# Kernel optimization log

Measured on AMD Instinct MI355X. Metric: run time of the kernel, lower is better.

The kernel has to match this reference:

```python
import jax, jax.numpy as jnp
import numpy as np

N = 40000          # nodes
E = 640000         # edges (avg degree 16)
D_MODEL = 128
H = 8              # num_heads
DH = 16            # d_head
DFF = 512
CLAMP = 5.0
EPS = 1e-5


def setup_inputs() -> dict:
    key = jax.random.key(0)
    ks = jax.random.split(key, 10)
    s = 0.08  # weight init scale
    return {
        "feat": jax.random.normal(ks[0], (N, D_MODEL), dtype=jnp.float32),
        "src": jax.random.randint(ks[1], (E,), 0, N, dtype=jnp.int32),
        "dst": jax.random.randint(ks[2], (E,), 0, N, dtype=jnp.int32),
        "Wq": jax.random.normal(ks[3], (H * DH, D_MODEL), dtype=jnp.float32) * s,
        "Wk": jax.random.normal(ks[4], (H * DH, D_MODEL), dtype=jnp.float32) * s,
        "Wv": jax.random.normal(ks[5], (H * DH, D_MODEL), dtype=jnp.float32) * s,
        "Wo": jax.random.normal(ks[6], (D_MODEL, H * DH), dtype=jnp.float32) * s,
        "ln1_g": jnp.ones((D_MODEL,), jnp.float32),
        "ln1_b": jnp.zeros((D_MODEL,), jnp.float32),
        "W1": jax.random.normal(ks[7], (DFF, D_MODEL), dtype=jnp.float32) * s,
        "b1": jnp.zeros((DFF,), jnp.float32),
        "W2": jax.random.normal(ks[8], (D_MODEL, DFF), dtype=jnp.float32) * s,
        "b2": jnp.zeros((D_MODEL,), jnp.float32),
        "ln2_g": jnp.ones((D_MODEL,), jnp.float32),
        "ln2_b": jnp.zeros((D_MODEL,), jnp.float32),
    }


def _layer_norm(x, g, b):
    mu = jnp.mean(x, axis=-1, keepdims=True)
    var = jnp.mean(jnp.square(x - mu), axis=-1, keepdims=True)
    return (x - mu) * jax.lax.rsqrt(var + EPS) * g + b


def reference(feat, src, dst, Wq, Wk, Wv, Wo, ln1_g, ln1_b, W1, b1, W2, b2, ln2_g, ln2_b):
    n = feat.shape[0]
    # Node-level projections (equivalent to DGL's per-edge Linear on gathered feats)
    q = (feat @ Wq.T).reshape(n, H, DH)
    k = (feat @ Wk.T).reshape(n, H, DH)
    v = (feat @ Wv.T).reshape(n, H, DH)

    # Per-edge multi-head attention logits: q[dst] . k[src] / sqrt(d_head), clamped
    u = jnp.sum(q[dst] * k[src], axis=-1) / np.sqrt(DH)   # [E, H]
    u = jnp.clip(u, -CLAMP, CLAMP)

    # Ragged edge-softmax over incoming edges of each dst node
    m = jax.ops.segment_max(u, dst, num_segments=n)        # [N, H]
    e = jnp.exp(u - m[dst])                                # [E, H]
    denom = jax.ops.segment_sum(e, dst, num_segments=n)    # [N, H]
    a = e / denom[dst]                                     # [E, H]

    # Weighted V scatter-reduce back to dst nodes
    av = (a[:, :, None] * v[src]).reshape(-1, H * DH)      # [E, H*DH]
    sum_av = jax.ops.segment_sum(av, dst, num_segments=n)  # [N, H*DH]
    uh = sum_av @ Wo.T                                     # [N, d_model]

    h1 = _layer_norm(feat + uh, ln1_g, ln1_b)
    ffn = jax.nn.relu(h1 @ W1.T + b1) @ W2.T + b2
    return _layer_norm(h1 + ffn, ln2_g, ln2_b)
```

## Files before the change

### kernel.cpp

```cpp
#include <hip/hip_runtime.h>

#define DM 128
#define DFF 512
#define CLAMP_V 5.0f
#define LN_EPS 1e-5f

typedef __attribute__((ext_vector_type(8))) short bf16x8;
typedef __attribute__((ext_vector_type(4))) float f32x4;
typedef __attribute__((ext_vector_type(2))) float f32x2;

__device__ __forceinline__ float b2f(ushort u) {
  union { uint u; float f; } x; x.u = ((uint)u) << 16; return x.f;
}
__device__ __forceinline__ ushort f2b(float f) {
  union { float f; uint u; } x; x.f = f;
  uint r = x.u + 0x7FFFu + ((x.u >> 16) & 1u);
  return (ushort)(r >> 16);
}
__device__ __forceinline__ f32x2 upk2(uint w) {
  union { uint u; float f; } a, b;
  a.u = w << 16; b.u = w & 0xFFFF0000u;
  f32x2 r; r[0] = a.f; r[1] = b.f; return r;
}

__global__ void k_prep(const float* __restrict__ feat,
                       const float* __restrict__ wq, const float* __restrict__ wk,
                       const float* __restrict__ wv, const float* __restrict__ wo,
                       const float* __restrict__ w1, const float* __restrict__ w2,
                       ushort* __restrict__ feat_bf, ushort* __restrict__ wbf,
                       const int* __restrict__ dst, int* __restrict__ deg,
                       int nf4, int castBlocks, int E) {
  if ((int)blockIdx.x >= castBlocks) {
    int e = ((int)blockIdx.x - castBlocks) * 256 + threadIdx.x;
    if (e < E) atomicAdd(&deg[dst[e]], 1);
    return;
  }
  int i = blockIdx.x * 256 + threadIdx.x;
  if (i < nf4) {
    float4 v = *reinterpret_cast<const float4*>(feat + i * 4);
    ushort4 o; o.x = f2b(v.x); o.y = f2b(v.y); o.z = f2b(v.z); o.w = f2b(v.w);
    *reinterpret_cast<ushort4*>(feat_bf + i * 4) = o;
    return;
  }
  int i4 = (i - nf4) * 4;
  if (i4 >= 196608) return;
  const float* s; int o;
  if      (i4 < 16384)  { s = wq; o = i4; }
  else if (i4 < 32768)  { s = wk; o = i4 - 16384; }
  else if (i4 < 49152)  { s = wv; o = i4 - 32768; }
  else if (i4 < 65536)  { s = wo; o = i4 - 49152; }
  else if (i4 < 131072) { s = w1; o = i4 - 65536; }
  else                  { s = w2; o = i4 - 131072; }
  float4 v = *reinterpret_cast<const float4*>(s + o);
  ushort4 u; u.x = f2b(v.x); u.y = f2b(v.y); u.z = f2b(v.z); u.w = f2b(v.w);
  *reinterpret_cast<ushort4*>(wbf + i4) = u;
}

#define SC_EPB 1024

__global__ __launch_bounds__(256) void k_scan(const int* __restrict__ deg,
                                              int* __restrict__ off,
                                              int* __restrict__ cur,
                                              int n, int E) {
  __shared__ int sh[256];
  __shared__ int wsum[4];
  const int t = threadIdx.x;
  const int bstart = blockIdx.x * SC_EPB;

  int gs = 0;
  for (int base = t * 4; base < bstart; base += SC_EPB) {
    int4 v = *reinterpret_cast<const int4*>(deg + base);
    gs += v.x + v.y + v.z + v.w;
  }
  #pragma unroll
  for (int m = 1; m < 64; m <<= 1) gs += __shfl_xor(gs, m);
  if ((t & 63) == 0) wsum[t >> 6] = gs;
  __syncthreads();
  int gadd = wsum[0] + wsum[1] + wsum[2] + wsum[3];
  __syncthreads();

  int base = bstart + t * 4;
  int4 v = {0, 0, 0, 0};
  if (base + 3 < n) {
    v = *reinterpret_cast<const int4*>(deg + base);
  } else {
    if (base     < n) v.x = deg[base];
    if (base + 1 < n) v.y = deg[base + 1];
    if (base + 2 < n) v.z = deg[base + 2];
    if (base + 3 < n) v.w = deg[base + 3];
  }
  int s = v.x + v.y + v.z + v.w;
  sh[t] = s;
  __syncthreads();
  #pragma unroll
  for (int d = 1; d < 256; d <<= 1) {
    int x = 0;
    if (t >= d) x = sh[t - d];
    __syncthreads();
    sh[t] += x;
    __syncthreads();
  }
  int ex = sh[t] - s + gadd;
  if (base + 3 < n) {
    int4 o; o.x = ex; o.y = ex + v.x; o.z = ex + v.x + v.y; o.w = ex + v.x + v.y + v.z;
    *reinterpret_cast<int4*>(off + base) = o;
    int4 z = {0, 0, 0, 0};
    *reinterpret_cast<int4*>(cur + base) = z;
  } else {
    if (base     < n) { off[base]     = ex;                    cur[base]     = 0; }
    if (base + 1 < n) { off[base + 1] = ex + v.x;              cur[base + 1] = 0; }
    if (base + 2 < n) { off[base + 2] = ex + v.x + v.y;        cur[base + 2] = 0; }
    if (base + 3 < n) { off[base + 3] = ex + v.x + v.y + v.z;  cur[base + 3] = 0; }
  }
  if (blockIdx.x == 0 && t == 0) off[n] = E;
}

__global__ void k_scatter(const int* __restrict__ src, const int* __restrict__ dst,
                          const int* __restrict__ off, int* __restrict__ cur,
                          int* __restrict__ csr, int E) {
  int e = blockIdx.x * blockDim.x + threadIdx.x;
  if (e < E) {
    int d = dst[e];
    int p = off[d] + atomicAdd(&cur[d], 1);
    csr[p] = src[e];
  }
}

__global__ __launch_bounds__(512, 2) void k_qkv(
    const ushort* __restrict__ A, const ushort* __restrict__ W,
    ushort* __restrict__ Cb, ushort* __restrict__ Cb2, int M)
{
  __shared__ ushort As[128 * 128];
  __shared__ ushort Bs[128 * 128];

  const int tid = threadIdx.x;
  const int wv = tid >> 6, ln = tid & 63;
  const int bnb = blockIdx.x;
  const int mbase = blockIdx.y * 128;
  const int wrow = (wv >> 2) * 64, wcol = (wv & 3) * 32;
  const int o_base = tid * 16;

  #pragma unroll
  for (int is = 0; is < 4; ++is) {
    int o = is * 8192 + o_base;
    int row = o >> 8;
    int c = ((o >> 4) & 15) ^ (row & 15);
    int gr = min(mbase + row, M - 1);
    const ushort* sA = A + (size_t)gr * 128 + c * 8;
    __builtin_amdgcn_global_load_lds(
        (const __attribute__((address_space(1))) void*)sA,
        (__attribute__((address_space(3))) void*)((char*)As + is * 8192 + wv * 1024),
        16, 0, 0);
    const ushort* sB = W + (size_t)(bnb * 128 + row) * 128 + c * 8;
    __builtin_amdgcn_global_load_lds(
        (const __attribute__((address_space(1))) void*)sB,
        (__attribute__((address_space(3))) void*)((char*)Bs + is * 8192 + wv * 1024),
        16, 0, 0);
  }
  __syncthreads();

  f32x4 acc[4][2] = {};
  const char* AsB = (const char*)As;
  const char* BsB = (const char*)Bs;
  #pragma unroll
  for (int kk = 0; kk < 4; ++kk) {
    bf16x8 af[4], bfr[2];
    #pragma unroll
    for (int m = 0; m < 4; ++m) {
      int r = wrow + m * 16 + (ln & 15);
      int c = kk * 4 + (ln >> 4);
      af[m] = *reinterpret_cast<const bf16x8*>(AsB + r * 256 + ((c ^ (r & 15)) << 4));
    }
    #pragma unroll
    for (int n = 0; n < 2; ++n) {
      int r = wcol + n * 16 + (ln & 15);
      int c = kk * 4 + (ln >> 4);
      bfr[n] = *reinterpret_cast<const bf16x8*>(BsB + r * 256 + ((c ^ (r & 15)) << 4));
    }
    #pragma unroll
    for (int m = 0; m < 4; ++m)
      #pragma unroll
      for (int n = 0; n < 2; ++n)
        acc[m][n] = __builtin_amdgcn_mfma_f32_16x16x32_bf16(af[m], bfr[n], acc[m][n], 0, 0, 0);
  }

  #pragma unroll
  for (int m = 0; m < 4; ++m) {
    int gr0 = mbase + wrow + m * 16 + (ln >> 4) * 4;
    #pragma unroll
    for (int n = 0; n < 2; ++n) {
      int gcl = wcol + n * 16 + (ln & 15);
      #pragma unroll
      for (int r = 0; r < 4; ++r) {
        int gr = gr0 + r;
        if (gr >= M) continue;
        float v = acc[m][n][r];
        if (bnb == 0) Cb[(size_t)gr * 128 + gcl] = f2b(v);
        else          Cb2[(size_t)gr * 256 + (bnb - 1) * 128 + gcl] = f2b(v);
      }
    }
  }
}

__global__ __launch_bounds__(512, 2) void k_mmT(
    const ushort* __restrict__ A, const ushort* __restrict__ W,
    const float* __restrict__ res,
    const float* __restrict__ lng, const float* __restrict__ lnbv,
    ushort* __restrict__ Cb, int M)
{
  __shared__ ushort As[128 * 128];
  __shared__ ushort Bs[128 * 128];
  __shared__ float lnred[1024];

  const int tid = threadIdx.x;
  const int wv = tid >> 6, ln = tid & 63;
  const int mbase = blockIdx.y * 128;
  const int wrow = (wv >> 2) * 64, wcol = (wv & 3) * 32;
  const int o_base = tid * 16;

  #pragma unroll
  for (int is = 0; is < 4; ++is) {
    int o = is * 8192 + o_base;
    int row = o >> 8;
    int c = ((o >> 4) & 15) ^ (row & 15);
    int gr = min(mbase + row, M - 1);
    const ushort* sA = A + (size_t)gr * 128 + c * 8;
    __builtin_amdgcn_global_load_lds(
        (const __attribute__((address_space(1))) void*)sA,
        (__attribute__((address_space(3))) void*)((char*)As + is * 8192 + wv * 1024),
        16, 0, 0);
    const ushort* sB = W + (size_t)row * 128 + c * 8;
    __builtin_amdgcn_global_load_lds(
        (const __attribute__((address_space(1))) void*)sB,
        (__attribute__((address_space(3))) void*)((char*)Bs + is * 8192 + wv * 1024),
        16, 0, 0);
  }
  __syncthreads();

  f32x4 acc[4][2] = {};
  const char* AsB = (const char*)As;
  const char* BsB = (const char*)Bs;
  #pragma unroll
  for (int kk = 0; kk < 4; ++kk) {
    bf16x8 af[4], bfr[2];
    #pragma unroll
    for (int m = 0; m < 4; ++m) {
      int r = wrow + m * 16 + (ln & 15);
      int c = kk * 4 + (ln >> 4);
      af[m] = *reinterpret_cast<const bf16x8*>(AsB + r * 256 + ((c ^ (r & 15)) << 4));
    }
    #pragma unroll
    for (int n = 0; n < 2; ++n) {
      int r = wcol + n * 16 + (ln & 15);
      int c = kk * 4 + (ln >> 4);
      bfr[n] = *reinterpret_cast<const bf16x8*>(BsB + r * 256 + ((c ^ (r & 15)) << 4));
    }
    #pragma unroll
    for (int m = 0; m < 4; ++m)
      #pragma unroll
      for (int n = 0; n < 2; ++n)
        acc[m][n] = __builtin_amdgcn_mfma_f32_16x16x32_bf16(af[m], bfr[n], acc[m][n], 0, 0, 0);
  }

  #pragma unroll
  for (int m = 0; m < 4; ++m)
    #pragma unroll
    for (int n = 0; n < 2; ++n) {
      int gc = wcol + n * 16 + (ln & 15);
      #pragma unroll
      for (int r = 0; r < 4; ++r) {
        int gr = mbase + wrow + m * 16 + (ln >> 4) * 4 + r;
        acc[m][n][r] += res[(size_t)min(gr, M - 1) * 128 + gc];
      }
    }
  #pragma unroll
  for (int m = 0; m < 4; ++m)
    #pragma unroll
    for (int r = 0; r < 4; ++r) {
      float sm = acc[m][0][r] + acc[m][1][r];
      float sq = acc[m][0][r] * acc[m][0][r] + acc[m][1][r] * acc[m][1][r];
      #pragma unroll
      for (int msk = 1; msk <= 8; msk <<= 1) {
        sm += __shfl_xor(sm, msk);
        sq += __shfl_xor(sq, msk);
      }
      if ((ln & 15) == 0) {
        int row = wrow + m * 16 + (ln >> 4) * 4 + r;
        lnred[row * 8 + (wv & 3) * 2]     = sm;
        lnred[row * 8 + (wv & 3) * 2 + 1] = sq;
      }
    }
  __syncthreads();
  #pragma unroll
  for (int m = 0; m < 4; ++m)
    #pragma unroll
    for (int r = 0; r < 4; ++r) {
      int row = wrow + m * 16 + (ln >> 4) * 4 + r;
      int gr = mbase + row;
      float sm = lnred[row * 8] + lnred[row * 8 + 2] + lnred[row * 8 + 4] + lnred[row * 8 + 6];
      float sq = lnred[row * 8 + 1] + lnred[row * 8 + 3] + lnred[row * 8 + 5] + lnred[row * 8 + 7];
      float mu = sm * (1.f / 128.f);
      float var = fmaxf(sq * (1.f / 128.f) - mu * mu, 0.f);
      float rstd = rsqrtf(var + LN_EPS);
      if (gr < M) {
        #pragma unroll
        for (int n = 0; n < 2; ++n) {
          int gc = wcol + n * 16 + (ln & 15);
          float y = (acc[m][n][r] - mu) * rstd * lng[gc] + lnbv[gc];
          Cb[(size_t)gr * 128 + gc] = f2b(y);
        }
      }
    }
}

__global__ __launch_bounds__(512, 4) void k_ffn(
    const ushort* __restrict__ h1b,
    const ushort* __restrict__ w1, const float* __restrict__ b1,
    const ushort* __restrict__ w2, const float* __restrict__ b2,
    const float* __restrict__ lng, const float* __restrict__ lnbv,
    float* __restrict__ outp, int M)
{
  __shared__ ushort mid[32 * 512];
  __shared__ ushort wbuf[2][128 * 64];
  __shared__ float lnred[32 * 16];

  const int tid = threadIdx.x;
  const int wv = tid >> 6, ln = tid & 63;
  const int lr = ln & 15, hi = ln >> 4;
  const int mbase = blockIdx.x * 32;
  const int gc = wv * 16 + lr;

  auto STG64 = [&](const ushort* srcBase, int srcLd, int colOff, char* dstLds) {
    #pragma unroll
    for (int is = 0; is < 2; ++is) {
      int o = is * 8192 + tid * 16;
      int r = o >> 7;
      int c = ((o >> 4) & 7) ^ (r & 7);
      const ushort* s = srcBase + (size_t)r * srcLd + colOff + c * 8;
      __builtin_amdgcn_global_load_lds(
          (const __attribute__((address_space(1))) void*)s,
          (__attribute__((address_space(3))) void*)(dstLds + is * 8192 + wv * 1024),
          16, 0, 0);
    }
  };

  {
    int o = tid * 16;
    int r = o >> 8;
    int c = ((o >> 4) & 15) ^ (r & 15);
    int gr = min(mbase + r, M - 1);
    const ushort* s = h1b + (size_t)gr * 128 + c * 8;
    __builtin_amdgcn_global_load_lds(
        (const __attribute__((address_space(1))) void*)s,
        (__attribute__((address_space(3))) void*)((char*)mid + wv * 1024),
        16, 0, 0);
  }
  STG64(w1, 128, 0, (char*)wbuf[0]);
  __syncthreads();

  f32x4 p1[4][2] = {};
  const char* hB = (const char*)mid;
  #pragma unroll
  for (int g = 0; g < 4; ++g) {
    #pragma unroll
    for (int kh = 0; kh < 2; ++kh) {
      const int step = g * 2 + kh;
      if (step < 7) {
        int ns = step + 1;
        STG64(w1 + (size_t)(ns >> 1) * 128 * 128, 128, (ns & 1) * 64, (char*)wbuf[ns & 1]);
      } else {
        STG64(w2, 512, 0, (char*)wbuf[0]);
      }
      const char* wB = (const char*)wbuf[step & 1];
      #pragma unroll
      for (int kk = 0; kk < 2; ++kk) {
        int ct = kk * 4 + hi;
        int cg = kh * 8 + ct;
        int wr = wv * 16 + lr;
        bf16x8 aW = *reinterpret_cast<const bf16x8*>(wB + wr * 128 + ((ct ^ (wr & 7)) << 4));
        bf16x8 bH[2];
        #pragma unroll
        for (int hj = 0; hj < 2; ++hj) {
          int r = hj * 16 + lr;
          bH[hj] = *reinterpret_cast<const bf16x8*>(hB + r * 256 + ((cg ^ (r & 15)) << 4));
        }
        #pragma unroll
        for (int hj = 0; hj < 2; ++hj)
          p1[g][hj] = __builtin_amdgcn_mfma_f32_16x16x32_bf16(aW, bH[hj], p1[g][hj], 0, 0, 0);
      }
      __syncthreads();
    }
  }

  float h1res[2][4];
  {
    int chunk = gc >> 3;
    int sub = (gc & 7) * 2;
    #pragma unroll
    for (int m = 0; m < 2; ++m)
      #pragma unroll
      for (int r = 0; r < 4; ++r) {
        int row = m * 16 + hi * 4 + r;
        h1res[m][r] = b2f(*reinterpret_cast<const ushort*>(
            (const char*)mid + row * 256 + ((chunk ^ (row & 15)) << 4) + sub));
      }
  }
  __syncthreads();

  #pragma unroll
  for (int g = 0; g < 4; ++g) {
    int mc0 = g * 128 + wv * 16 + hi * 4;
    float4 bv = *reinterpret_cast<const float4*>(b1 + mc0);
    int chunk = mc0 >> 3;
    int sub = (mc0 & 7) * 2;
    #pragma unroll
    for (int hj = 0; hj < 2; ++hj) {
      int orow = hj * 16 + lr;
      ushort4 pk;
      pk.x = f2b(fmaxf(p1[g][hj][0] + bv.x, 0.f));
      pk.y = f2b(fmaxf(p1[g][hj][1] + bv.y, 0.f));
      pk.z = f2b(fmaxf(p1[g][hj][2] + bv.z, 0.f));
      pk.w = f2b(fmaxf(p1[g][hj][3] + bv.w, 0.f));
      char* dstp = (char*)mid + orow * 1024 + (((chunk & 63) ^ (orow & 15)) << 4) + sub;
      *reinterpret_cast<ushort4*>(dstp) = pk;
    }
  }
  __syncthreads();

  f32x4 p2[2] = {};
  #pragma unroll
  for (int kt = 0; kt < 8; ++kt) {
    if (kt < 7) STG64(w2, 512, (kt + 1) * 64, (char*)wbuf[(kt + 1) & 1]);
    const char* wB = (const char*)wbuf[kt & 1];
    #pragma unroll
    for (int kk = 0; kk < 2; ++kk) {
      int ct = kk * 4 + hi;
      int cm = kt * 8 + ct;
      int wr = wv * 16 + lr;
      bf16x8 bW = *reinterpret_cast<const bf16x8*>(wB + wr * 128 + ((ct ^ (wr & 7)) << 4));
      bf16x8 aM[2];
      #pragma unroll
      for (int m = 0; m < 2; ++m) {
        int r = m * 16 + lr;
        aM[m] = *reinterpret_cast<const bf16x8*>((const char*)mid + r * 1024 + (((cm & 63) ^ (r & 15)) << 4));
      }
      #pragma unroll
      for (int m = 0; m < 2; ++m)
        p2[m] = __builtin_amdgcn_mfma_f32_16x16x32_bf16(aM[m], bW, p2[m], 0, 0, 0);
    }
    __syncthreads();
  }

  {
    float bsv = b2[gc];
    #pragma unroll
    for (int m = 0; m < 2; ++m)
      #pragma unroll
      for (int r = 0; r < 4; ++r)
        p2[m][r] += bsv + h1res[m][r];
  }
  #pragma unroll
  for (int m = 0; m < 2; ++m)
    #pragma unroll
    for (int r = 0; r < 4; ++r) {
      float sm = p2[m][r];
      float sq = p2[m][r] * p2[m][r];
      #pragma unroll
      for (int msk = 1; msk <= 8; msk <<= 1) {
        sm += __shfl_xor(sm, msk);
        sq += __shfl_xor(sq, msk);
      }
      if (lr == 0) {
        int row = m * 16 + hi * 4 + r;
        lnred[row * 16 + wv * 2]     = sm;
        lnred[row * 16 + wv * 2 + 1] = sq;
      }
    }
  __syncthreads();
  {
    float g2v = lng[gc], bb2 = lnbv[gc];
    #pragma unroll
    for (int m = 0; m < 2; ++m)
      #pragma unroll
      for (int r = 0; r < 4; ++r) {
        int row = m * 16 + hi * 4 + r;
        int gr = mbase + row;
        float sm = 0.f, sq = 0.f;
        #pragma unroll
        for (int w = 0; w < 8; ++w) {
          sm += lnred[row * 16 + w * 2];
          sq += lnred[row * 16 + w * 2 + 1];
        }
        float mu = sm * (1.f / 128.f);
        float var = fmaxf(sq * (1.f / 128.f) - mu * mu, 0.f);
        float rstd = rsqrtf(var + LN_EPS);
        if (gr < M)
          outp[(size_t)gr * 128 + gc] = (p2[m][r] - mu) * rstd * g2v + bb2;
      }
  }
}

__global__ __launch_bounds__(256) void k_attn(
    const ushort* __restrict__ q, const ushort* __restrict__ kv,
    const int* __restrict__ off, const int* __restrict__ csr,
    ushort* __restrict__ sav, int n)
{
  int node = blockIdx.x * 4 + (threadIdx.x >> 6);
  int lane = threadIdx.x & 63;
  if (node >= n) return;
  const int g = lane >> 3, sl = lane & 7;

  const ushort* qr = q + (size_t)node * 128 + sl * 16;
  uint4 qw0 = *reinterpret_cast<const uint4*>(qr);
  uint4 qw1 = *reinterpret_cast<const uint4*>(qr + 8);
  f32x2 qv[8];
  qv[0] = upk2(qw0.x); qv[1] = upk2(qw0.y); qv[2] = upk2(qw0.z); qv[3] = upk2(qw0.w);
  qv[4] = upk2(qw1.x); qv[5] = upk2(qw1.y); qv[6] = upk2(qw1.z); qv[7] = upk2(qw1.w);

  int b = off[node], e = off[node + 1];
  float s = 0.f;
  f32x2 a2[8] = {};
  int nIt = (e - b + 7) >> 3;
  int idx = b + g;
  int sn = (b < e) ? csr[min(idx, e - 1)] : 0;

  for (int i = 0; i < nIt; ++i) {
    bool act = idx < e;
    const ushort* kr = kv + (size_t)sn * 256 + sl * 16;
    uint4 kw0 = *reinterpret_cast<const uint4*>(kr);
    uint4 kw1 = *reinterpret_cast<const uint4*>(kr + 8);
    uint4 vw0 = *reinterpret_cast<const uint4*>(kr + 128);
    uint4 vw1 = *reinterpret_cast<const uint4*>(kr + 136);
    idx += 8;
    if (i + 1 < nIt) sn = csr[min(idx, e - 1)];

    f32x2 acc = qv[0] * upk2(kw0.x);
    acc += qv[1] * upk2(kw0.y);
    acc += qv[2] * upk2(kw0.z);
    acc += qv[3] * upk2(kw0.w);
    acc += qv[4] * upk2(kw1.x);
    acc += qv[5] * upk2(kw1.y);
    acc += qv[6] * upk2(kw1.z);
    acc += qv[7] * upk2(kw1.w);
    float p = acc[0] + acc[1];
    float u = fminf(fmaxf(p * 0.25f, -CLAMP_V), CLAMP_V);
    float w = __expf(u - CLAMP_V);
    w = act ? w : 0.f;
    s += w;
    f32x2 w2v; w2v[0] = w; w2v[1] = w;
    a2[0] += w2v * upk2(vw0.x);
    a2[1] += w2v * upk2(vw0.y);
    a2[2] += w2v * upk2(vw0.z);
    a2[3] += w2v * upk2(vw0.w);
    a2[4] += w2v * upk2(vw1.x);
    a2[5] += w2v * upk2(vw1.y);
    a2[6] += w2v * upk2(vw1.z);
    a2[7] += w2v * upk2(vw1.w);
  }

  #pragma unroll
  for (int msk = 8; msk <= 32; msk <<= 1) {
    s += __shfl_xor(s, msk);
    #pragma unroll
    for (int j = 0; j < 8; ++j) {
      a2[j][0] += __shfl_xor(a2[j][0], msk);
      a2[j][1] += __shfl_xor(a2[j][1], msk);
    }
  }

  float inv = (s > 0.f) ? 1.f / s : 0.f;
  if (g == 0) {
    uint w[8];
    #pragma unroll
    for (int j = 0; j < 8; ++j)
      w[j] = (uint)f2b(a2[j][0] * inv) | ((uint)f2b(a2[j][1] * inv) << 16);
    ushort* outp = sav + (size_t)node * 128 + sl * 16;
    uint4 o0 = {w[0], w[1], w[2], w[3]};
    uint4 o1 = {w[4], w[5], w[6], w[7]};
    *reinterpret_cast<uint4*>(outp) = o0;
    *reinterpret_cast<uint4*>(outp + 8) = o1;
  }
}

extern "C" void kernel_launch(void* const* d_in, const int* in_sizes, int n_in,
                              void* d_out, int out_size, void* d_ws, size_t ws_size,
                              hipStream_t stream)
{
  const float* feat = (const float*)d_in[0];
  const int*   src  = (const int*)d_in[1];
  const int*   dst  = (const int*)d_in[2];
  const float* Wq   = (const float*)d_in[3];
  const float* Wk   = (const float*)d_in[4];
  const float* Wv   = (const float*)d_in[5];
  const float* Wo   = (const float*)d_in[6];
  const float* ln1g = (const float*)d_in[7];
  const float* ln1b = (const float*)d_in[8];
  const float* W1   = (const float*)d_in[9];
  const float* b1   = (const float*)d_in[10];
  const float* W2   = (const float*)d_in[11];
  const float* b2   = (const float*)d_in[12];
  const float* ln2g = (const float*)d_in[13];
  const float* ln2b = (const float*)d_in[14];
  float* out = (float*)d_out;

  const int N = in_sizes[0] / DM;
  const int E = in_sizes[1];
  const size_t NB = (size_t)N;

  char* wsb = (char*)d_ws;
  ushort* q_bf    = (ushort*)wsb;
  ushort* kv_bf   = (ushort*)(wsb + NB * 256);
  ushort* sav_bf  = (ushort*)(wsb + NB * 768);
  ushort* h1b     = (ushort*)(wsb + NB * 1536);
  ushort* feat_bf = (ushort*)(wsb + NB * 1792);
  ushort* wbf     = (ushort*)(wsb + NB * 2048);
  ushort* wqkv_bf = wbf;
  ushort* wo_bf   = wbf + 49152;
  ushort* w1_bf   = wbf + 65536;
  ushort* w2_bf   = wbf + 131072;
  int* ib  = (int*)(wbf + 196608);
  int* deg = ib;
  int* cur = ib + N;
  int* off = ib + 2 * N;
  int* csr = ib + 3 * N + 1;

  hipMemsetAsync(deg, 0, (size_t)N * sizeof(int), stream);

  int nf4 = N * DM / 4;
  int castBlocks = (nf4 + 49152 + 255) / 256;
  int cntBlocks = (E + 255) / 256;
  k_prep<<<castBlocks + cntBlocks, 256, 0, stream>>>(
      feat, Wq, Wk, Wv, Wo, W1, W2, feat_bf, wbf, dst, deg, nf4, castBlocks, E);

  int nbk = (N + SC_EPB - 1) / SC_EPB;
  k_scan<<<nbk, 256, 0, stream>>>(deg, off, cur, N, E);
  k_scatter<<<cntBlocks, 256, 0, stream>>>(src, dst, off, cur, csr, E);

  const int nT = (N + 127) / 128;
  k_qkv<<<dim3(3, nT), 512, 0, stream>>>(feat_bf, wqkv_bf, q_bf, kv_bf, N);

  int nb4 = (N + 3) / 4;
  k_attn<<<nb4, 256, 0, stream>>>(q_bf, kv_bf, off, csr, sav_bf, N);

  k_mmT<<<dim3(1, nT), 512, 0, stream>>>(sav_bf, wo_bf, feat, ln1g, ln1b, h1b, N);

  const int nF = (N + 31) / 32;
  k_ffn<<<nF, 512, 0, stream>>>(
      h1b, w1_bf, b1, w2_bf, b2, ln2g, ln2b, out, N);
}
```

Baseline: 190.6 us.

## Fuse edge attention with output projection and first LayerNorm

Merges the per-node attention aggregation kernel with the Wo projection, residual add and LayerNorm kernel. Each 512-thread block handles 32 nodes, keeps the aggregated values in a swizzled LDS tile, loads Wo into LDS, and applies MFMA plus LN before writing h1. This removes one launch and the global write and re-read of the intermediate attention output. In exchange, each block loads the full Wo tile for only 32 rows, and the attention loop runs four nodes per wave sequentially, which may lower occupancy and memory-level parallelism.

```diff
diff --git a/kernel.cpp b/kernel.cpp
--- a/kernel.cpp
+++ b/kernel.cpp
@@ -202,115 +202,176 @@
   }
 }
 
-__global__ __launch_bounds__(512, 2) void k_mmT(
-    const ushort* __restrict__ A, const ushort* __restrict__ W,
-    const float* __restrict__ res,
-    const float* __restrict__ lng, const float* __restrict__ lnbv,
-    ushort* __restrict__ Cb, int M)
+__global__ __launch_bounds__(512, 2) void k_attn(
+    const ushort* __restrict__ q, const ushort* __restrict__ kv,
+    const int* __restrict__ off, const int* __restrict__ csr,
+    const float* __restrict__ feat, const ushort* __restrict__ wo,
+    const float* __restrict__ ln1g, const float* __restrict__ ln1b,
+    ushort* __restrict__ h1b, int n)
 {
-  __shared__ ushort As[128 * 128];
-  __shared__ ushort Bs[128 * 128];
-  __shared__ float lnred[1024];
+  __shared__ ushort savt[32 * 128];
+  __shared__ ushort wot[128 * 128];
+  __shared__ float lnred[32 * 16];
 
   const int tid = threadIdx.x;
   const int wv = tid >> 6, ln = tid & 63;
-  const int mbase = blockIdx.y * 128;
-  const int wrow = (wv >> 2) * 64, wcol = (wv & 3) * 32;
-  const int o_base = tid * 16;
+  const int lr = ln & 15, hi = ln >> 4;
+  const int g = ln >> 3, sl = ln & 7;
+  const int mbase = blockIdx.x * 32;
 
   #pragma unroll
   for (int is = 0; is < 4; ++is) {
-    int o = is * 8192 + o_base;
-    int row = o >> 8;
-    int c = ((o >> 4) & 15) ^ (row & 15);
-    int gr = min(mbase + row, M - 1);
-    const ushort* sA = A + (size_t)gr * 128 + c * 8;
+    int o = is * 8192 + tid * 16;
+    int r = o >> 8;
+    int c = ((o >> 4) & 15) ^ (r & 15);
+    const ushort* s = wo + (size_t)r * 128 + c * 8;
     __builtin_amdgcn_global_load_lds(
-        (const __attribute__((address_space(1))) void*)sA,
-        (__attribute__((address_space(3))) void*)((char*)As + is * 8192 + wv * 1024),
+        (const __attribute__((address_space(1))) void*)s,
+        (__attribute__((address_space(3))) void*)((char*)wot + is * 8192 + wv * 1024),
         16, 0, 0);
-    const ushort* sB = W + (size_t)row * 128 + c * 8;
-    __builtin_amdgcn_global_load_lds(
-        (const __attribute__((address_space(1))) void*)sB,
-        (__attribute__((address_space(3))) void*)((char*)Bs + is * 8192 + wv * 1024),
-        16, 0, 0);
-  }
-  __syncthreads();
-
-  f32x4 acc[4][2] = {};
-  const char* AsB = (const char*)As;
-  const char* BsB = (const char*)Bs;
+  }
+
+  for (int i = 0; i < 4; ++i) {
+    int node = mbase + wv * 4 + i;
+    if (node < n) {
+      const ushort* qr = q + (size_t)node * 128 + sl * 16;
+      uint4 qw0 = *reinterpret_cast<const uint4*>(qr);
+      uint4 qw1 = *reinterpret_cast<const uint4*>(qr + 8);
+      f32x2 qv[8];
+      qv[0] = upk2(qw0.x); qv[1] = upk2(qw0.y); qv[2] = upk2(qw0.z); qv[3] = upk2(qw0.w);
+      qv[4] = upk2(qw1.x); qv[5] = upk2(qw1.y); qv[6] = upk2(qw1.z); qv[7] = upk2(qw1.w);
+
+      int b = off[node], e = off[node + 1];
+      float s = 0.f;
+      f32x2 a2[8] = {};
+      int nIt = (e - b + 7) >> 3;
+      int idx = b + g;
+      int sn = (b < e) ? csr[min(idx, e - 1)] : 0;
+
+      for (int it = 0; it < nIt; ++it) {
+        bool act = idx < e;
+        const ushort* kr = kv + (size_t)sn * 256 + sl * 16;
+        uint4 kw0 = *reinterpret_cast<const uint4*>(kr);
+        uint4 kw1 = *reinterpret_cast<const uint4*>(kr + 8);
+        uint4 vw0 = *reinterpret_cast<const uint4*>(kr + 128);
+        uint4 vw1 = *reinterpret_cast<const uint4*>(kr + 136);
+        idx += 8;
+        if (it + 1 < nIt) sn = csr[min(idx, e - 1)];
+
+        f32x2 acc = qv[0] * upk2(kw0.x);
+        acc += qv[1] * upk2(kw0.y);
+        acc += qv[2] * upk2(kw0.z);
+        acc += qv[3] * upk2(kw0.w);
+        acc += qv[4] * upk2(kw1.x);
+        acc += qv[5] * upk2(kw1.y);
+        acc += qv[6] * upk2(kw1.z);
+        acc += qv[7] * upk2(kw1.w);
+        float p = acc[0] + acc[1];
+        float u = fminf(fmaxf(p * 0.25f, -CLAMP_V), CLAMP_V);
+        float w = __expf(u - CLAMP_V);
+        w = act ? w : 0.f;
+        s += w;
+        f32x2 w2v; w2v[0] = w; w2v[1] = w;
+        a2[0] += w2v * upk2(vw0.x);
+        a2[1] += w2v * upk2(vw0.y);
+        a2[2] += w2v * upk2(vw0.z);
+        a2[3] += w2v * upk2(vw0.w);
+        a2[4] += w2v * upk2(vw1.x);
+        a2[5] += w2v * upk2(vw1.y);
+        a2[6] += w2v * upk2(vw1.z);
+        a2[7] += w2v * upk2(vw1.w);
+      }
+
+      #pragma unroll
+      for (int msk = 8; msk <= 32; msk <<= 1) {
+        s += __shfl_xor(s, msk);
+        #pragma unroll
+        for (int j = 0; j < 8; ++j) {
+          a2[j][0] += __shfl_xor(a2[j][0], msk);
+          a2[j][1] += __shfl_xor(a2[j][1], msk);
+        }
+      }
+
+      float inv = (s > 0.f) ? 1.f / s : 0.f;
+      if (g == 0) {
+        uint w[8];
+        #pragma unroll
+        for (int j = 0; j < 8; ++j)
+          w[j] = (uint)f2b(a2[j][0] * inv) | ((uint)f2b(a2[j][1] * inv) << 16);
+        int nl = wv * 4 + i;
+        int c0 = sl * 2, c1 = sl * 2 + 1;
+        uint4 o0 = {w[0], w[1], w[2], w[3]};
+        uint4 o1 = {w[4], w[5], w[6], w[7]};
+        *reinterpret_cast<uint4*>((char*)savt + nl * 256 + ((c0 ^ (nl & 15)) << 4)) = o0;
+        *reinterpret_cast<uint4*>((char*)savt + nl * 256 + ((c1 ^ (nl & 15)) << 4)) = o1;
+      }
+    }
+  }
+  __syncthreads();
+
+  const int gc = wv * 16 + lr;
+  f32x4 p0[2] = {};
   #pragma unroll
   for (int kk = 0; kk < 4; ++kk) {
-    bf16x8 af[4], bfr[2];
-    #pragma unroll
-    for (int m = 0; m < 4; ++m) {
-      int r = wrow + m * 16 + (ln & 15);
-      int c = kk * 4 + (ln >> 4);
-      af[m] = *reinterpret_cast<const bf16x8*>(AsB + r * 256 + ((c ^ (r & 15)) << 4));
-    }
-    #pragma unroll
-    for (int n = 0; n < 2; ++n) {
-      int r = wcol + n * 16 + (ln & 15);
-      int c = kk * 4 + (ln >> 4);
-      bfr[n] = *reinterpret_cast<const bf16x8*>(BsB + r * 256 + ((c ^ (r & 15)) << 4));
-    }
-    #pragma unroll
-    for (int m = 0; m < 4; ++m)
-      #pragma unroll
-      for (int n = 0; n < 2; ++n)
-        acc[m][n] = __builtin_amdgcn_mfma_f32_16x16x32_bf16(af[m], bfr[n], acc[m][n], 0, 0, 0);
-  }
-
-  #pragma unroll
-  for (int m = 0; m < 4; ++m)
-    #pragma unroll
-    for (int n = 0; n < 2; ++n) {
-      int gc = wcol + n * 16 + (ln & 15);
-      #pragma unroll
-      for (int r = 0; r < 4; ++r) {
-        int gr = mbase + wrow + m * 16 + (ln >> 4) * 4 + r;
-        acc[m][n][r] += res[(size_t)min(gr, M - 1) * 128 + gc];
-      }
-    }
-  #pragma unroll
-  for (int m = 0; m < 4; ++m)
+    int c = kk * 4 + hi;
+    int wr = wv * 16 + lr;
+    bf16x8 bWo = *reinterpret_cast<const bf16x8*>((char*)wot + wr * 256 + ((c ^ (wr & 15)) << 4));
+    bf16x8 aS[2];
+    #pragma unroll
+    for (int m = 0; m < 2; ++m) {
+      int r = m * 16 + lr;
+      aS[m] = *reinterpret_cast<const bf16x8*>((char*)savt + r * 256 + ((c ^ (r & 15)) << 4));
+    }
+    #pragma unroll
+    for (int m = 0; m < 2; ++m)
+      p0[m] = __builtin_amdgcn_mfma_f32_16x16x32_bf16(aS[m], bWo, p0[m], 0, 0, 0);
+  }
+  #pragma unroll
+  for (int m = 0; m < 2; ++m)
     #pragma unroll
     for (int r = 0; r < 4; ++r) {
-      float sm = acc[m][0][r] + acc[m][1][r];
-      float sq = acc[m][0][r] * acc[m][0][r] + acc[m][1][r] * acc[m][1][r];
+      int gr = mbase + m * 16 + hi * 4 + r;
+      p0[m][r] += feat[(size_t)min(gr, n - 1) * 128 + gc];
+    }
+  #pragma unroll
+  for (int m = 0; m < 2; ++m)
+    #pragma unroll
+    for (int r = 0; r < 4; ++r) {
+      float sm = p0[m][r];
+      float sq = p0[m][r] * p0[m][r];
       #pragma unroll
       for (int msk = 1; msk <= 8; msk <<= 1) {
         sm += __shfl_xor(sm, msk);
         sq += __shfl_xor(sq, msk);
       }
-      if ((ln & 15) == 0) {
-        int row = wrow + m * 16 + (ln >> 4) * 4 + r;
-        lnred[row * 8 + (wv & 3) * 2]     = sm;
-        lnred[row * 8 + (wv & 3) * 2 + 1] = sq;
-      }
-    }
-  __syncthreads();
-  #pragma unroll
-  for (int m = 0; m < 4; ++m)
-    #pragma unroll
-    for (int r = 0; r < 4; ++r) {
-      int row = wrow + m * 16 + (ln >> 4) * 4 + r;
-      int gr = mbase + row;
-      float sm = lnred[row * 8] + lnred[row * 8 + 2] + lnred[row * 8 + 4] + lnred[row * 8 + 6];
-      float sq = lnred[row * 8 + 1] + lnred[row * 8 + 3] + lnred[row * 8 + 5] + lnred[row * 8 + 7];
-      float mu = sm * (1.f / 128.f);
-      float var = fmaxf(sq * (1.f / 128.f) - mu * mu, 0.f);
-      float rstd = rsqrtf(var + LN_EPS);
-      if (gr < M) {
+      if (lr == 0) {
+        int row = m * 16 + hi * 4 + r;
+        lnred[row * 16 + wv * 2]     = sm;
+        lnred[row * 16 + wv * 2 + 1] = sq;
+      }
+    }
+  __syncthreads();
+  {
+    float g1v = ln1g[gc], bb1 = ln1b[gc];
+    #pragma unroll
+    for (int m = 0; m < 2; ++m)
+      #pragma unroll
+      for (int r = 0; r < 4; ++r) {
+        int row = m * 16 + hi * 4 + r;
+        int gr = mbase + row;
+        float sm = 0.f, sq = 0.f;
         #pragma unroll
-        for (int n = 0; n < 2; ++n) {
-          int gc = wcol + n * 16 + (ln & 15);
-          float y = (acc[m][n][r] - mu) * rstd * lng[gc] + lnbv[gc];
-          Cb[(size_t)gr * 128 + gc] = f2b(y);
+        for (int w = 0; w < 8; ++w) {
+          sm += lnred[row * 16 + w * 2];
+          sq += lnred[row * 16 + w * 2 + 1];
         }
-      }
-    }
+        float mu = sm * (1.f / 128.f);
+        float var = fmaxf(sq * (1.f / 128.f) - mu * mu, 0.f);
+        float rstd = rsqrtf(var + LN_EPS);
+        if (gr < n)
+          h1b[(size_t)gr * 128 + gc] = f2b((p0[m][r] - mu) * rstd * g1v + bb1);
+      }
+  }
 }
 
 __global__ __launch_bounds__(512, 4) void k_ffn(
@@ -497,88 +558,6 @@
         if (gr < M)
           outp[(size_t)gr * 128 + gc] = (p2[m][r] - mu) * rstd * g2v + bb2;
       }
-  }
-}
-
-__global__ __launch_bounds__(256) void k_attn(
-    const ushort* __restrict__ q, const ushort* __restrict__ kv,
-    const int* __restrict__ off, const int* __restrict__ csr,
-    ushort* __restrict__ sav, int n)
-{
-  int node = blockIdx.x * 4 + (threadIdx.x >> 6);
-  int lane = threadIdx.x & 63;
-  if (node >= n) return;
-  const int g = lane >> 3, sl = lane & 7;
-
-  const ushort* qr = q + (size_t)node * 128 + sl * 16;
-  uint4 qw0 = *reinterpret_cast<const uint4*>(qr);
-  uint4 qw1 = *reinterpret_cast<const uint4*>(qr + 8);
-  f32x2 qv[8];
-  qv[0] = upk2(qw0.x); qv[1] = upk2(qw0.y); qv[2] = upk2(qw0.z); qv[3] = upk2(qw0.w);
-  qv[4] = upk2(qw1.x); qv[5] = upk2(qw1.y); qv[6] = upk2(qw1.z); qv[7] = upk2(qw1.w);
-
-  int b = off[node], e = off[node + 1];
-  float s = 0.f;
-  f32x2 a2[8] = {};
-  int nIt = (e - b + 7) >> 3;
-  int idx = b + g;
-  int sn = (b < e) ? csr[min(idx, e - 1)] : 0;
-
-  for (int i = 0; i < nIt; ++i) {
-    bool act = idx < e;
-    const ushort* kr = kv + (size_t)sn * 256 + sl * 16;
-    uint4 kw0 = *reinterpret_cast<const uint4*>(kr);
-    uint4 kw1 = *reinterpret_cast<const uint4*>(kr + 8);
-    uint4 vw0 = *reinterpret_cast<const uint4*>(kr + 128);
-    uint4 vw1 = *reinterpret_cast<const uint4*>(kr + 136);
-    idx += 8;
-    if (i + 1 < nIt) sn = csr[min(idx, e - 1)];
-
-    f32x2 acc = qv[0] * upk2(kw0.x);
-    acc += qv[1] * upk2(kw0.y);
-    acc += qv[2] * upk2(kw0.z);
-    acc += qv[3] * upk2(kw0.w);
-    acc += qv[4] * upk2(kw1.x);
-    acc += qv[5] * upk2(kw1.y);
-    acc += qv[6] * upk2(kw1.z);
-    acc += qv[7] * upk2(kw1.w);
-    float p = acc[0] + acc[1];
-    float u = fminf(fmaxf(p * 0.25f, -CLAMP_V), CLAMP_V);
-    float w = __expf(u - CLAMP_V);
-    w = act ? w : 0.f;
-    s += w;
-    f32x2 w2v; w2v[0] = w; w2v[1] = w;
-    a2[0] += w2v * upk2(vw0.x);
-    a2[1] += w2v * upk2(vw0.y);
-    a2[2] += w2v * upk2(vw0.z);
-    a2[3] += w2v * upk2(vw0.w);
-    a2[4] += w2v * upk2(vw1.x);
-    a2[5] += w2v * upk2(vw1.y);
-    a2[6] += w2v * upk2(vw1.z);
-    a2[7] += w2v * upk2(vw1.w);
-  }
-
-  #pragma unroll
-  for (int msk = 8; msk <= 32; msk <<= 1) {
-    s += __shfl_xor(s, msk);
-    #pragma unroll
-    for (int j = 0; j < 8; ++j) {
-      a2[j][0] += __shfl_xor(a2[j][0], msk);
-      a2[j][1] += __shfl_xor(a2[j][1], msk);
-    }
-  }
-
-  float inv = (s > 0.f) ? 1.f / s : 0.f;
-  if (g == 0) {
-    uint w[8];
-    #pragma unroll
-    for (int j = 0; j < 8; ++j)
-      w[j] = (uint)f2b(a2[j][0] * inv) | ((uint)f2b(a2[j][1] * inv) << 16);
-    ushort* outp = sav + (size_t)node * 128 + sl * 16;
-    uint4 o0 = {w[0], w[1], w[2], w[3]};
-    uint4 o1 = {w[4], w[5], w[6], w[7]};
-    *reinterpret_cast<uint4*>(outp) = o0;
-    *reinterpret_cast<uint4*>(outp + 8) = o1;
   }
 }
 
@@ -610,7 +589,6 @@
   char* wsb = (char*)d_ws;
   ushort* q_bf    = (ushort*)wsb;
   ushort* kv_bf   = (ushort*)(wsb + NB * 256);
-  ushort* sav_bf  = (ushort*)(wsb + NB * 768);
   ushort* h1b     = (ushort*)(wsb + NB * 1536);
   ushort* feat_bf = (ushort*)(wsb + NB * 1792);
   ushort* wbf     = (ushort*)(wsb + NB * 2048);
@@ -639,10 +617,9 @@
   const int nT = (N + 127) / 128;
   k_qkv<<<dim3(3, nT), 512, 0, stream>>>(feat_bf, wqkv_bf, q_bf, kv_bf, N);
 
-  int nb4 = (N + 3) / 4;
-  k_attn<<<nb4, 256, 0, stream>>>(q_bf, kv_bf, off, csr, sav_bf, N);
-
-  k_mmT<<<dim3(1, nT), 512, 0, stream>>>(sav_bf, wo_bf, feat, ln1g, ln1b, h1b, N);
+  const int nA = (N + 31) / 32;
+  k_attn<<<nA, 512, 0, stream>>>(
+      q_bf, kv_bf, off, csr, feat, wo_bf, ln1g, ln1b, h1b, N);
 
   const int nF = (N + 31) / 32;
   k_ffn<<<nF, 512, 0, stream>>>(
```

Result: no change. 189.5 us (median of 2 runs) (-0.6%).
